# Kernel optimization log

Hardware: AMD Instinct MI355X
Metric: run time of the kernel (lower is better)

## Reference

```python
import jax, jax.numpy as jnp
import numpy as np

BEAM_WIDTH = 5  # degenerate: all beams share the same per-step topk, so best beam == greedy argmax path
BLANK = 0


def setup_inputs() -> dict:
    key = jax.random.key(0)
    N, C, T = 128, 128, 2048
    logits = jax.random.normal(key, (N, C, T), dtype=jnp.float32)
    return {"logits": logits}


def reference(logits) -> jnp.ndarray:
    # (N, C, T) -> (N, T, C), log-softmax over classes (matches F.log_softmax(dim=2))
    log_probs = jax.nn.log_softmax(jnp.transpose(logits, (0, 2, 1)), axis=2)
    N, T, C = log_probs.shape
    # Beam search in the source is degenerate: every beam expands with the identical
    # per-timestep top-k, so the highest-scoring beam is exactly the per-step argmax.
    tokens = jnp.argmax(log_probs, axis=2).astype(jnp.int32)  # (N, T)
    # CTC-style collapse (decode()): drop blanks and repeated tokens.
    prev = jnp.concatenate([jnp.full((N, 1), -1, dtype=jnp.int32), tokens[:, :-1]], axis=1)
    keep = (tokens != BLANK) & (tokens != prev)  # (N, T) bool
    # Left-compact kept tokens into a blank-padded (N, T) output.
    pos = jnp.cumsum(keep, axis=1) - 1            # target position if kept
    pos = jnp.where(keep, pos, T)                 # dropped tokens -> dump slot T
    out = jnp.full((N, T + 1), BLANK, dtype=jnp.int32)
    out = out.at[jnp.arange(N)[:, None], pos].set(tokens)
    return out[:, :T]
```

## Files before the change

kernel.cpp:

```cpp
#include <hip/hip_runtime.h>


constexpr int N = 128;
constexpr int C = 128;
constexpr int T = 2048;

__global__ __launch_bounds__(256) void argmax_kernel(const float* __restrict__ logits,
                                                     int* __restrict__ tokens) {
    const int gid = blockIdx.x * blockDim.x + threadIdx.x;
    const int n  = gid / (T / 4);
    const int t4 = (gid % (T / 4)) * 4;
    const float* base = logits + (size_t)n * C * T + t4;

    float4 best = *(const float4*)(base);
    int4 bidx = make_int4(0, 0, 0, 0);
    #pragma unroll 4
    for (int c = 1; c < C; ++c) {
        float4 v = *(const float4*)(base + (size_t)c * T);
        if (v.x > best.x) { best.x = v.x; bidx.x = c; }
        if (v.y > best.y) { best.y = v.y; bidx.y = c; }
        if (v.z > best.z) { best.z = v.z; bidx.z = c; }
        if (v.w > best.w) { best.w = v.w; bidx.w = c; }
    }
    *(int4*)(tokens + (size_t)n * T + t4) = bidx;
}

__global__ __launch_bounds__(256) void collapse_kernel(const int* __restrict__ tokens,
                                                       int* __restrict__ out) {
    const int n = blockIdx.x;
    const int* trow = tokens + (size_t)n * T;
    int* orow = out + (size_t)n * T;
    const int tid = threadIdx.x;
    constexpr int PER = T / 256;
    const int t0 = tid * PER;

    int tok[PER];
    *(int4*)&tok[0] = *(const int4*)(trow + t0);
    *(int4*)&tok[4] = *(const int4*)(trow + t0 + 4);
    int prev = (t0 == 0) ? -1 : trow[t0 - 1];

    int kpos[PER];
    int cnt = 0;
    #pragma unroll
    for (int i = 0; i < PER; ++i) {
        const bool k = (tok[i] != 0) && (tok[i] != prev);
        kpos[i] = k ? cnt : -1;
        cnt += k ? 1 : 0;
        prev = tok[i];
    }

    const int lane = tid & 63;
    const int wid  = tid >> 6;
    int incl = cnt;
    #pragma unroll
    for (int d = 1; d < 64; d <<= 1) {
        int v = __shfl_up(incl, d, 64);
        if (lane >= d) incl += v;
    }

    __shared__ int wsum[4];
    if (lane == 63) wsum[wid] = incl;

    const int4 z = make_int4(0, 0, 0, 0);
    *(int4*)(orow + t0)     = z;
    *(int4*)(orow + t0 + 4) = z;

    __syncthreads();

    int wbase = 0;
    #pragma unroll
    for (int w = 0; w < 4; ++w)
        if (w < wid) wbase += wsum[w];
    const int base = wbase + (incl - cnt);

    #pragma unroll
    for (int i = 0; i < PER; ++i) {
        if (kpos[i] >= 0) orow[base + kpos[i]] = tok[i];
    }
}

extern "C" void kernel_launch(void* const* d_in, const int* in_sizes, int n_in,
                              void* d_out, int out_size, void* d_ws, size_t ws_size,
                              hipStream_t stream) {
    const float* logits = (const float*)d_in[0];
    int* out = (int*)d_out;
    int* tokens = (int*)d_ws;

    const int threadsA = 256;
    const int gridA = (N * T / 4) / threadsA;
    argmax_kernel<<<gridA, threadsA, 0, stream>>>(logits, tokens);
    collapse_kernel<<<N, 256, 0, stream>>>(tokens, out);
}
```

Baseline: 32.43 us.

## Split argmax class reduction across two thread halves with shared-memory merge

Each argmax block now assigns two thread halves to the two 64-class halves for the same 512 time steps, then merges the partial maxima through shared memory. This doubles the number of threads and in-flight loads while halving each thread's serial loop, aiming to better saturate HBM bandwidth. It adds a block barrier and shared-memory traffic, and half the threads sit idle during the final write.

```diff
diff --git a/kernel.cpp b/kernel.cpp
--- a/kernel.cpp
+++ b/kernel.cpp
@@ -7,22 +7,43 @@
 
 __global__ __launch_bounds__(256) void argmax_kernel(const float* __restrict__ logits,
                                                      int* __restrict__ tokens) {
-    const int gid = blockIdx.x * blockDim.x + threadIdx.x;
-    const int n  = gid / (T / 4);
-    const int t4 = (gid % (T / 4)) * 4;
-    const float* base = logits + (size_t)n * C * T + t4;
+    __shared__ float sbest[128][4];
+    __shared__ int   sidx[128][4];
+
+    const int tid  = threadIdx.x;
+    const int tq   = tid & 127;
+    const int half = tid >> 7;
+    const int blk  = blockIdx.x;
+    const int n    = blk >> 2;
+    const int t4   = ((blk & 3) * 128 + tq) * 4;
+
+    const float* base = logits + (size_t)n * C * T + (size_t)(half * 64) * T + t4;
 
     float4 best = *(const float4*)(base);
     int4 bidx = make_int4(0, 0, 0, 0);
-    #pragma unroll 4
-    for (int c = 1; c < C; ++c) {
+    #pragma unroll 8
+    for (int c = 1; c < 64; ++c) {
         float4 v = *(const float4*)(base + (size_t)c * T);
         if (v.x > best.x) { best.x = v.x; bidx.x = c; }
         if (v.y > best.y) { best.y = v.y; bidx.y = c; }
         if (v.z > best.z) { best.z = v.z; bidx.z = c; }
         if (v.w > best.w) { best.w = v.w; bidx.w = c; }
     }
-    *(int4*)(tokens + (size_t)n * T + t4) = bidx;
+
+    if (half) {
+        sbest[tq][0] = best.x; sbest[tq][1] = best.y;
+        sbest[tq][2] = best.z; sbest[tq][3] = best.w;
+        sidx[tq][0] = bidx.x + 64; sidx[tq][1] = bidx.y + 64;
+        sidx[tq][2] = bidx.z + 64; sidx[tq][3] = bidx.w + 64;
+    }
+    __syncthreads();
+    if (!half) {
+        if (sbest[tq][0] > best.x) bidx.x = sidx[tq][0];
+        if (sbest[tq][1] > best.y) bidx.y = sidx[tq][1];
+        if (sbest[tq][2] > best.z) bidx.z = sidx[tq][2];
+        if (sbest[tq][3] > best.w) bidx.w = sidx[tq][3];
+        *(int4*)(tokens + (size_t)n * T + t4) = bidx;
+    }
 }
 
 __global__ __launch_bounds__(256) void collapse_kernel(const int* __restrict__ tokens,
@@ -86,8 +107,7 @@
     int* out = (int*)d_out;
     int* tokens = (int*)d_ws;
 
-    const int threadsA = 256;
-    const int gridA = (N * T / 4) / threadsA;
-    argmax_kernel<<<gridA, threadsA, 0, stream>>>(logits, tokens);
+    const int gridA = N * 4;
+    argmax_kernel<<<gridA, 256, 0, stream>>>(logits, tokens);
     collapse_kernel<<<N, 256, 0, stream>>>(tokens, out);
 }
```

Result: faster. 27.44 us (-15.4%).

## Fuse argmax and collapse into one cooperative kernel with split-class reduction

Applied to the files above, without the earlier changes.

Merges the two launches into a single cooperative kernel that does the argmax, then a grid-wide sync, then the CTC collapse. Each block now covers 256 timesteps, with its four wavefronts each scanning 32 classes and merging the partial maxima through shared memory. This shortens the per-thread serial loop and removes a kernel launch boundary. In exchange it adds a grid barrier, requires all 1024 blocks to be co-resident, and leaves most blocks idle during the collapse phase.

```diff
diff --git a/kernel.cpp b/kernel.cpp
--- a/kernel.cpp
+++ b/kernel.cpp
@@ -1,36 +1,64 @@
 #include <hip/hip_runtime.h>
+#include <hip/hip_cooperative_groups.h>
+
+namespace coop = cooperative_groups;
 
 
 constexpr int N = 128;
 constexpr int C = 128;
 constexpr int T = 2048;
 
-__global__ __launch_bounds__(256) void argmax_kernel(const float* __restrict__ logits,
-                                                     int* __restrict__ tokens) {
-    const int gid = blockIdx.x * blockDim.x + threadIdx.x;
-    const int n  = gid / (T / 4);
-    const int t4 = (gid % (T / 4)) * 4;
-    const float* base = logits + (size_t)n * C * T + t4;
+__global__ __launch_bounds__(256) void fused_kernel(const float* __restrict__ logits,
+                                                    int* __restrict__ tokens,
+                                                    int* __restrict__ out) {
+    __shared__ float sb[3][64][4];
+    __shared__ int   si[3][64][4];
+
+    const int tid = threadIdx.x;
+    const int tq  = tid & 63;
+    const int grp = tid >> 6;
+    const int b   = blockIdx.x;
+    const int n   = b >> 3;
+    const int t4  = (b & 7) * 256 + tq * 4;
+
+    const float* base = logits + (size_t)n * C * T + (size_t)(grp * 32) * T + t4;
 
     float4 best = *(const float4*)(base);
     int4 bidx = make_int4(0, 0, 0, 0);
-    #pragma unroll 4
-    for (int c = 1; c < C; ++c) {
+    #pragma unroll 8
+    for (int c = 1; c < 32; ++c) {
         float4 v = *(const float4*)(base + (size_t)c * T);
         if (v.x > best.x) { best.x = v.x; bidx.x = c; }
         if (v.y > best.y) { best.y = v.y; bidx.y = c; }
         if (v.z > best.z) { best.z = v.z; bidx.z = c; }
         if (v.w > best.w) { best.w = v.w; bidx.w = c; }
     }
-    *(int4*)(tokens + (size_t)n * T + t4) = bidx;
-}
 
-__global__ __launch_bounds__(256) void collapse_kernel(const int* __restrict__ tokens,
-                                                       int* __restrict__ out) {
-    const int n = blockIdx.x;
-    const int* trow = tokens + (size_t)n * T;
-    int* orow = out + (size_t)n * T;
-    const int tid = threadIdx.x;
+    if (grp > 0) {
+        *(float4*)sb[grp - 1][tq] = best;
+        int4 gi = make_int4(bidx.x + grp * 32, bidx.y + grp * 32,
+                            bidx.z + grp * 32, bidx.w + grp * 32);
+        *(int4*)si[grp - 1][tq] = gi;
+    }
+    __syncthreads();
+    if (grp == 0) {
+        #pragma unroll
+        for (int g = 0; g < 3; ++g) {
+            float4 ob = *(float4*)sb[g][tq];
+            int4   oi = *(int4*)si[g][tq];
+            if (ob.x > best.x) { best.x = ob.x; bidx.x = oi.x; }
+            if (ob.y > best.y) { best.y = ob.y; bidx.y = oi.y; }
+            if (ob.z > best.z) { best.z = ob.z; bidx.z = oi.z; }
+            if (ob.w > best.w) { best.w = ob.w; bidx.w = oi.w; }
+        }
+        *(int4*)(tokens + (size_t)n * T + t4) = bidx;
+    }
+
+    coop::this_grid().sync();
+
+    if (b >= N) return;
+    const int* trow = tokens + (size_t)b * T;
+    int* orow = out + (size_t)b * T;
     constexpr int PER = T / 256;
     const int t0 = tid * PER;
 
@@ -71,11 +99,11 @@
     #pragma unroll
     for (int w = 0; w < 4; ++w)
         if (w < wid) wbase += wsum[w];
-    const int base = wbase + (incl - cnt);
+    const int base2 = wbase + (incl - cnt);
 
     #pragma unroll
     for (int i = 0; i < PER; ++i) {
-        if (kpos[i] >= 0) orow[base + kpos[i]] = tok[i];
+        if (kpos[i] >= 0) orow[base2 + kpos[i]] = tok[i];
     }
 }
 
@@ -86,8 +114,7 @@
     int* out = (int*)d_out;
     int* tokens = (int*)d_ws;
 
-    const int threadsA = 256;
-    const int gridA = (N * T / 4) / threadsA;
-    argmax_kernel<<<gridA, threadsA, 0, stream>>>(logits, tokens);
-    collapse_kernel<<<N, 256, 0, stream>>>(tokens, out);
+    void* args[] = { (void*)&logits, (void*)&tokens, (void*)&out };
+    hipLaunchCooperativeKernel((const void*)fused_kernel,
+                               dim3(N * 8), dim3(256), args, 0, stream);
 }
```

New measurement: 125.2 us. +286.0%, slower.

## Split argmax class dimension across four wavefronts with shared-memory reduction

Applied to the files above, without the earlier changes.

The argmax kernel now gives each 256-thread block 256 timesteps and splits the 128 classes into four groups of 32, one per wavefront. Each wave batches eight float4 loads before comparing, which raises memory-level parallelism. The partial maxima are merged through shared memory by wave 0. The grid stays the same size, but the per-thread serial chain gets shorter in exchange for a barrier and some LDS traffic. Ties keep the first index because lower groups are merged first with a strict greater-than.

```diff
diff --git a/kernel.cpp b/kernel.cpp
--- a/kernel.cpp
+++ b/kernel.cpp
@@ -7,22 +7,56 @@
 
 __global__ __launch_bounds__(256) void argmax_kernel(const float* __restrict__ logits,
                                                      int* __restrict__ tokens) {
-    const int gid = blockIdx.x * blockDim.x + threadIdx.x;
-    const int n  = gid / (T / 4);
-    const int t4 = (gid % (T / 4)) * 4;
-    const float* base = logits + (size_t)n * C * T + t4;
+    __shared__ float sb[3][4][64];
+    __shared__ int   si[3][4][64];
 
-    float4 best = *(const float4*)(base);
+    const int tid = threadIdx.x;
+    const int tq  = tid & 63;
+    const int grp = tid >> 6;
+    const int b   = blockIdx.x;
+    const int n   = b >> 3;
+    const int t4  = (b & 7) * 256 + tq * 4;
+
+    const float* base = logits + (size_t)n * C * T + (size_t)(grp * 32) * T + t4;
+
+    float4 best = make_float4(-__builtin_inff(), -__builtin_inff(),
+                              -__builtin_inff(), -__builtin_inff());
     int4 bidx = make_int4(0, 0, 0, 0);
-    #pragma unroll 4
-    for (int c = 1; c < C; ++c) {
-        float4 v = *(const float4*)(base + (size_t)c * T);
-        if (v.x > best.x) { best.x = v.x; bidx.x = c; }
-        if (v.y > best.y) { best.y = v.y; bidx.y = c; }
-        if (v.z > best.z) { best.z = v.z; bidx.z = c; }
-        if (v.w > best.w) { best.w = v.w; bidx.w = c; }
+
+    #pragma unroll
+    for (int cc = 0; cc < 32; cc += 8) {
+        float4 v[8];
+        #pragma unroll
+        for (int j = 0; j < 8; ++j)
+            v[j] = *(const float4*)(base + (size_t)(cc + j) * T);
+        #pragma unroll
+        for (int j = 0; j < 8; ++j) {
+            const int c = cc + j;
+            if (v[j].x > best.x) { best.x = v[j].x; bidx.x = c; }
+            if (v[j].y > best.y) { best.y = v[j].y; bidx.y = c; }
+            if (v[j].z > best.z) { best.z = v[j].z; bidx.z = c; }
+            if (v[j].w > best.w) { best.w = v[j].w; bidx.w = c; }
+        }
     }
-    *(int4*)(tokens + (size_t)n * T + t4) = bidx;
+
+    if (grp > 0) {
+        sb[grp - 1][0][tq] = best.x; si[grp - 1][0][tq] = bidx.x + grp * 32;
+        sb[grp - 1][1][tq] = best.y; si[grp - 1][1][tq] = bidx.y + grp * 32;
+        sb[grp - 1][2][tq] = best.z; si[grp - 1][2][tq] = bidx.z + grp * 32;
+        sb[grp - 1][3][tq] = best.w; si[grp - 1][3][tq] = bidx.w + grp * 32;
+    }
+    __syncthreads();
+    if (grp == 0) {
+        #pragma unroll
+        for (int g = 0; g < 3; ++g) {
+            float f;
+            f = sb[g][0][tq]; if (f > best.x) { best.x = f; bidx.x = si[g][0][tq]; }
+            f = sb[g][1][tq]; if (f > best.y) { best.y = f; bidx.y = si[g][1][tq]; }
+            f = sb[g][2][tq]; if (f > best.z) { best.z = f; bidx.z = si[g][2][tq]; }
+            f = sb[g][3][tq]; if (f > best.w) { best.w = f; bidx.w = si[g][3][tq]; }
+        }
+        *(int4*)(tokens + (size_t)n * T + t4) = bidx;
+    }
 }
 
 __global__ __launch_bounds__(256) void collapse_kernel(const int* __restrict__ tokens,
@@ -71,11 +105,11 @@
     #pragma unroll
     for (int w = 0; w < 4; ++w)
         if (w < wid) wbase += wsum[w];
-    const int base = wbase + (incl - cnt);
+    const int base2 = wbase + (incl - cnt);
 
     #pragma unroll
     for (int i = 0; i < PER; ++i) {
-        if (kpos[i] >= 0) orow[base + kpos[i]] = tok[i];
+        if (kpos[i] >= 0) orow[base2 + kpos[i]] = tok[i];
     }
 }
 
@@ -86,8 +120,6 @@
     int* out = (int*)d_out;
     int* tokens = (int*)d_ws;
 
-    const int threadsA = 256;
-    const int gridA = (N * T / 4) / threadsA;
-    argmax_kernel<<<gridA, threadsA, 0, stream>>>(logits, tokens);
+    argmax_kernel<<<N * 8, 256, 0, stream>>>(logits, tokens);
     collapse_kernel<<<N, 256, 0, stream>>>(tokens, out);
 }
```

After: 27.76 us. 14.4% less time.
